# Kernel optimization log

Hardware: AMD Instinct MI355X
Metric: run time of the kernel (lower is better)

## Reference

```python
import jax, jax.numpy as jnp
import numpy as np

D_MODEL, D_HEAD, D_MLP, N_HEADS = 768, 64, 3072, 12
BATCH, SEQ = 1, 4096
LN_EPS = 1e-05
IGNORE = -100000.0


def setup_inputs() -> dict:
    key = jax.random.key(0)
    ks = jax.random.split(key, 8)
    s = 0.02
    return {
        "resid_pre": jax.random.normal(ks[0], (BATCH, SEQ, D_MODEL), jnp.float32),
        "ln1_w": jnp.ones((D_MODEL,), jnp.float32),
        "ln1_b": jnp.zeros((D_MODEL,), jnp.float32),
        "ln2_w": jnp.ones((D_MODEL,), jnp.float32),
        "ln2_b": jnp.zeros((D_MODEL,), jnp.float32),
        "W_Q": jax.random.normal(ks[1], (N_HEADS, D_MODEL, D_HEAD), jnp.float32) * s,
        "W_K": jax.random.normal(ks[2], (N_HEADS, D_MODEL, D_HEAD), jnp.float32) * s,
        "W_V": jax.random.normal(ks[3], (N_HEADS, D_MODEL, D_HEAD), jnp.float32) * s,
        "W_O": jax.random.normal(ks[4], (N_HEADS, D_HEAD, D_MODEL), jnp.float32) * s,
        "b_Q": jnp.zeros((N_HEADS, D_HEAD), jnp.float32),
        "b_K": jnp.zeros((N_HEADS, D_HEAD), jnp.float32),
        "b_V": jnp.zeros((N_HEADS, D_HEAD), jnp.float32),
        "b_O": jnp.zeros((D_MODEL,), jnp.float32),
        "W_in": jax.random.normal(ks[5], (D_MODEL, D_MLP), jnp.float32) * s,
        "b_in": jnp.zeros((D_MLP,), jnp.float32),
        "W_out": jax.random.normal(ks[6], (D_MLP, D_MODEL), jnp.float32) * s,
        "b_out": jnp.zeros((D_MODEL,), jnp.float32),
    }


def _layernorm(x, w, b):
    mean = jnp.mean(x, axis=-1, keepdims=True)
    var = jnp.var(x, axis=-1, keepdims=True)  # unbiased=False
    return (x - mean) * jax.lax.rsqrt(var + LN_EPS) * w + b


def _attention(x, W_Q, W_K, W_V, W_O, b_Q, b_K, b_V, b_O):
    # x: [b, s, d_model]; W_{Q,K,V}: [h, d_model, d_head]
    q = jnp.einsum("bsm,hmd->bshd", x, W_Q) + b_Q
    k = jnp.einsum("bsm,hmd->bshd", x, W_K) + b_K
    v = jnp.einsum("bsm,hmd->bshd", x, W_V) + b_V
    scores = jnp.einsum("bqhd,bkhd->bhqk", q, k) / np.sqrt(D_HEAD).astype(np.float32)
    seq = x.shape[1]
    causal = jnp.tril(jnp.ones((seq, seq), bool))  # True where allowed
    scores = jnp.where(causal, scores, IGNORE)
    pattern = jax.nn.softmax(scores, axis=-1)
    z = jnp.einsum("bkhd,bhqk->bqhd", v, pattern)
    return jnp.einsum("bqhd,hdm->bqm", z, W_O) + b_O


def reference(resid_pre, ln1_w, ln1_b, ln2_w, ln2_b,
              W_Q, W_K, W_V, W_O, b_Q, b_K, b_V, b_O,
              W_in, b_in, W_out, b_out):
    resid_mid = _attention(_layernorm(resid_pre, ln1_w, ln1_b),
                           W_Q, W_K, W_V, W_O, b_Q, b_K, b_V, b_O) + resid_pre
    pre = jnp.einsum("bsm,mf->bsf", _layernorm(resid_mid, ln2_w, ln2_b), W_in) + b_in
    post = jax.nn.gelu(pre, approximate=False)  # torch F.gelu default = exact erf
    mlp_out = jnp.einsum("bsf,fm->bsm", post, W_out) + b_out
    resid_post = mlp_out + resid_mid
    return (resid_post, post)
```

## Files before the change

kernel.cpp:

```cpp
#include <hip/hip_runtime.h>
#include <hip/hip_bf16.h>
#include <math.h>

using bf16 = __hip_bfloat16;
using u16  = unsigned short;
using u32  = unsigned int;
using short8 = __attribute__((ext_vector_type(8))) short;
using f32x4  = __attribute__((ext_vector_type(4))) float;

#define AS1 __attribute__((address_space(1)))
#define AS3 __attribute__((address_space(3)))

__device__ __forceinline__ void gld_lds16(const void* g, void* l) {
  __builtin_amdgcn_global_load_lds((const AS1 u32*)g, (AS3 u32*)l, 16, 0, 0);
}

__device__ __forceinline__ bool probe_f32(const void* p) {
  return *(const u32*)p == 0x3F800000u;
}
__device__ __forceinline__ float ldf(const void* p, size_t i, bool f32) {
  return f32 ? ((const float*)p)[i] : __bfloat162float(((const bf16*)p)[i]);
}
__device__ __forceinline__ void stf(void* p, size_t i, float v, bool f32) {
  if (f32) ((float*)p)[i] = v;
  else     ((bf16*)p)[i] = __float2bfloat16(v);
}
__device__ __forceinline__ u32 cvt_pk_bf16(float lo, float hi) {
  u32 r;
  asm("v_cvt_pk_bf16_f32 %0, %1, %2" : "=v"(r) : "v"(lo), "v"(hi));
  return r;
}

__global__ __launch_bounds__(256) void ln_kernel(const void* __restrict__ x,
    const void* __restrict__ w, const void* __restrict__ b, bf16* __restrict__ out,
    const void* probe, int x_is_f32)
{
  const bool pf = probe_f32(probe);
  const bool xf = x_is_f32 ? true : pf;
  const int row = blockIdx.x, t = threadIdx.x;
  const size_t base = (size_t)row * 768;
  float v[3]; float s1 = 0.f, s2 = 0.f;
#pragma unroll
  for (int i = 0; i < 3; ++i) { float f = ldf(x, base + i*256 + t, xf); v[i] = f; s1 += f; s2 += f*f; }
#pragma unroll
  for (int off = 32; off >= 1; off >>= 1) { s1 += __shfl_xor(s1, off); s2 += __shfl_xor(s2, off); }
  __shared__ float a1[4], a2[4];
  if ((t & 63) == 0) { a1[t>>6] = s1; a2[t>>6] = s2; }
  __syncthreads();
  float S1 = a1[0]+a1[1]+a1[2]+a1[3];
  float S2 = a2[0]+a2[1]+a2[2]+a2[3];
  float mean = S1 * (1.f/768.f);
  float var  = S2 * (1.f/768.f) - mean*mean;
  float rs = rsqrtf(var + 1e-5f);
#pragma unroll
  for (int i = 0; i < 3; ++i) {
    int c = i*256 + t;
    out[base + c] = __float2bfloat16((v[i]-mean)*rs*ldf(w, c, pf) + ldf(b, c, pf));
  }
}

__global__ __launch_bounds__(256) void prep_all(
    const void* W_Q, const void* W_K, const void* W_V, const void* Wo,
    const void* Win, const void* Wout,
    const void* bQ, const void* bK, const void* bV, const void* bO,
    const void* bIn, const void* bOut,
    bf16* __restrict__ qkvT, bf16* __restrict__ WoT, bf16* __restrict__ WinT,
    bf16* __restrict__ WoutT, float* __restrict__ biasA,
    const void* __restrict__ xres, bf16* __restrict__ lnout, const void* probe)
{
  const bool pf = probe_f32(probe);
  const int bid = blockIdx.x;
  const int t = threadIdx.x;
  if (bid >= 6939) {
    const int row = bid - 6939;
    const size_t base = (size_t)row * 768;
    float v[3]; float s1 = 0.f, s2 = 0.f;
#pragma unroll
    for (int i = 0; i < 3; ++i) { float f = ldf(xres, base + i*256 + t, pf); v[i] = f; s1 += f; s2 += f*f; }
#pragma unroll
    for (int off = 32; off >= 1; off >>= 1) { s1 += __shfl_xor(s1, off); s2 += __shfl_xor(s2, off); }
    __shared__ float a1[4], a2[4];
    if ((t & 63) == 0) { a1[t>>6] = s1; a2[t>>6] = s2; }
    __syncthreads();
    float S1 = a1[0]+a1[1]+a1[2]+a1[3];
    float S2 = a2[0]+a2[1]+a2[2]+a2[3];
    float mean = S1 * (1.f/768.f);
    float var  = S2 * (1.f/768.f) - mean*mean;
    float rs = rsqrtf(var + 1e-5f);
#pragma unroll
    for (int i = 0; i < 3; ++i)
      lnout[base + i*256 + t] = __float2bfloat16((v[i]-mean)*rs);
    return;
  }
  if (bid >= 6912) {
    int i = (bid - 6912)*256 + t;
    float v;
    if (i < 2304)      v = (i < 768) ? ldf(bQ, i, pf) : (i < 1536 ? ldf(bK, i-768, pf) : ldf(bV, i-1536, pf));
    else if (i < 3072) v = ldf(bO, i-2304, pf);
    else if (i < 6144) v = ldf(bIn, i-3072, pf);
    else               v = ldf(bOut, i-6144, pf);
    biasA[i] = v;
    return;
  }
  const void* src; bf16* dst; int R, C, bx, by; size_t soff = 0;
  if (bid < 1728) {
    int mtx = bid / 576, within = bid % 576;
    int h = within / 48, tt = within % 48;
    by = tt >> 1; bx = tt & 1;
    src = (mtx == 0) ? W_Q : (mtx == 1 ? W_K : W_V);
    soff = (size_t)h * 49152;
    dst = qkvT + ((size_t)mtx*768 + h*64) * 768;
    R = 768; C = 64;
  } else if (bid < 2304) {
    int within = bid - 1728; bx = within % 24; by = within / 24;
    src = Wo; dst = WoT; R = 768; C = 768;
  } else if (bid < 4608) {
    int within = bid - 2304; bx = within % 96; by = within / 96;
    src = Win; dst = WinT; R = 768; C = 3072;
  } else {
    int within = bid - 4608; bx = within % 24; by = within / 24;
    src = Wout; dst = WoutT; R = 3072; C = 768;
  }
  __shared__ bf16 tile[32][33];
  const int bc = bx*32, br = by*32;
  const int tx = t & 31, ty = t >> 5;
#pragma unroll
  for (int i = 0; i < 32; i += 8)
    tile[ty+i][tx] = __float2bfloat16(ldf(src, soff + (size_t)(br+ty+i)*C + bc + tx, pf));
  __syncthreads();
#pragma unroll
  for (int i = 0; i < 32; i += 8)
    dst[(size_t)(bc+ty+i)*R + br + tx] = tile[tx][ty+i];
}


template<int MODE, int BM, int BN, int BK>
__global__ __launch_bounds__(256) void gemm_bt(const bf16* __restrict__ A,
    const bf16* __restrict__ BT, const float* __restrict__ bias,
    const void* __restrict__ res, void* __restrict__ Cout, bf16* __restrict__ aux,
    size_t outOff, const void* probe, int M, int N, int K,
    float* __restrict__ zf, float* __restrict__ sf)
{
  constexpr int MR = BM/32, NR = BN/32;
  constexpr int CH = BK/8;
  __shared__ bf16 Alds[BM*BK];
  __shared__ bf16 Blds[BN*BK];
  const int tid = threadIdx.x;
  const int lane = tid & 63, w = tid >> 6;
  const int l15 = lane & 15, l4 = lane >> 4;

  if (MODE == 0) {
    int bid = blockIdx.y * gridDim.x + blockIdx.x;
    float4 z4 = {0.f, 0.f, 0.f, 0.f};
    float4* zp = (float4*)zf + (size_t)bid*1024;
#pragma unroll
    for (int i = 0; i < 4; ++i) zp[i*256 + tid] = z4;
    if (tid < 16) ((float4*)sf)[bid*16 + tid] = z4;
  }

  const int brow = blockIdx.y * BM, bcol = blockIdx.x * BN;
  const int wr = (w >> 1) * (BM/2), wc = (w & 1) * (BN/2);
  const bf16* Ag = A  + (size_t)brow * K;
  const bf16* Bg = BT + (size_t)bcol * K;
  f32x4 acc[MR][NR];
#pragma unroll
  for (int i = 0; i < MR; ++i)
#pragma unroll
    for (int j = 0; j < NR; ++j) acc[i][j] = 0.f;

  for (int kt = 0; kt < K; kt += BK) {
#pragma unroll
    for (int i = 0; i < BM*CH/256; ++i) {
      int id = i*256 + tid, r = id / CH, cc = id % CH;
      int sw = (r ^ (r >> 3)) & 7;
      gld_lds16(Ag + (size_t)r*K + kt + ((cc ^ sw) * 8), (char*)Alds + id*16);
    }
#pragma unroll
    for (int i = 0; i < BN*CH/256; ++i) {
      int id = i*256 + tid, r = id / CH, cc = id % CH;
      int sw = (r ^ (r >> 3)) & 7;
      gld_lds16(Bg + (size_t)r*K + kt + ((cc ^ sw) * 8), (char*)Blds + id*16);
    }
    __syncthreads();
#pragma unroll
    for (int kk = 0; kk < BK/32; ++kk) {
      short8 a[MR], b[NR];
#pragma unroll
      for (int mi = 0; mi < MR; ++mi) {
        int row = wr + mi*16 + l15, sw = (row ^ (row >> 3)) & 7;
        a[mi] = *(const short8*)((const char*)Alds + row*(BK*2) + (((kk*4 + l4) ^ sw) << 4));
      }
#pragma unroll
      for (int ni = 0; ni < NR; ++ni) {
        int row = wc + ni*16 + l15, sw = (row ^ (row >> 3)) & 7;
        b[ni] = *(const short8*)((const char*)Blds + row*(BK*2) + (((kk*4 + l4) ^ sw) << 4));
      }
      __builtin_amdgcn_s_setprio(1);
#pragma unroll
      for (int mi = 0; mi < MR; ++mi)
#pragma unroll
        for (int ni = 0; ni < NR; ++ni)
          acc[mi][ni] = __builtin_amdgcn_mfma_f32_16x16x32_bf16(a[mi], b[ni], acc[mi][ni], 0, 0, 0);
      __builtin_amdgcn_s_setprio(0);
    }
    __syncthreads();
  }

  const bool pf = probe_f32(probe);
#pragma unroll
  for (int mi = 0; mi < MR; ++mi) {
#pragma unroll
    for (int r = 0; r < 4; ++r) {
      int row = brow + wr + mi*16 + l4*4 + r;
      size_t rowoff = (size_t)row * N;
#pragma unroll
      for (int ni = 0; ni < NR; ++ni) {
        int col = bcol + wc + ni*16 + l15;
        float v = acc[mi][ni][r] + bias[col];
        if (MODE == 1) v += ldf(res, rowoff + col, pf);
        if (MODE == 3) v += ((const float*)res)[rowoff + col];
        if (MODE == 2) v = 0.5f * v * (1.0f + erff(v * 0.70710678118654752f));
        if (MODE == 0) ((bf16*)Cout)[rowoff + col] = __float2bfloat16(v);
        else if (MODE == 1) ((float*)Cout)[rowoff + col] = v;
        else {
          stf(Cout, outOff + rowoff + col, v, pf);
          if (MODE == 2) aux[rowoff + col] = __float2bfloat16(v);
        }
      }
    }
  }
}

__global__ __launch_bounds__(256) void attn_kernel(const bf16* __restrict__ QKV,
    float* __restrict__ Zf, float* __restrict__ Sf)
{
  __shared__ bf16 Ks[2][4096];
  __shared__ bf16 VTs[2][4096];
  __shared__ bf16 Ps[4][1024];
  const int cid = 159 - blockIdx.x, h = blockIdx.y;
  int qb, c;
  if (cid < 16)      { qb = cid;                    c = 0; }
  else if (cid < 48) { qb = 16 + ((cid-16) >> 1);   c = (cid-16) & 1; }
  else if (cid < 96) { qb = 32 + (cid-48)/3;        c = (cid-48)%3; }
  else               { qb = 48 + ((cid-96) >> 2);   c = (cid-96) & 3; }
  const int t_lo = c*16, t_hi = min(c*16 + 16, qb + 1);

  const int tid = threadIdx.x, lane = tid & 63, w = tid >> 6;
  const int l15 = lane & 15, l4 = lane >> 4;
  const int q0 = qb * 64;

  short8 qf[2];
#pragma unroll
  for (int kk = 0; kk < 2; ++kk)
    qf[kk] = *(const short8*)(QKV + (size_t)(q0 + w*16 + l15)*2304 + h*64 + kk*32 + l4*8);

  int kaddr[2][4], vaddr[2][4], pst[4], pld[2], vwa[8];
#pragma unroll
  for (int kk = 0; kk < 2; ++kk)
#pragma unroll
    for (int ct = 0; ct < 4; ++ct) {
      int krow = ct*16 + l15, sk = (krow ^ (krow >> 3)) & 7;
      kaddr[kk][ct] = krow*128 + (((kk*4 + l4) ^ sk) << 4);
      vaddr[kk][ct] = kaddr[kk][ct];
    }
#pragma unroll
  for (int r = 0; r < 4; ++r) {
    int prow = l4*4 + r, sp = (prow ^ (prow >> 3)) & 7;
    pst[r] = prow*128 + (((l15 >> 1) ^ sp) << 4) + (l15 & 1)*8;
  }
#pragma unroll
  for (int kg = 0; kg < 2; ++kg) {
    int sp2 = (l15 ^ (l15 >> 3)) & 7;
    pld[kg] = l15*128 + (((kg*4 + l4) ^ sp2) << 4);
  }
  const int vw = tid >> 3, vd0 = (tid & 7) * 8;
  const int vk0 = (vw >> 1) + (vw & 1) * 32;
#pragma unroll
  for (int d = 0; d < 8; ++d) {
    int row = vd0 + d, srow = (row ^ (row >> 3)) & 7;
    vwa[d] = row*128 + (((vw >> 2) ^ srow) << 4) + (vw & 3)*4;
  }

  const ptrdiff_t STEP = 64*2304;
  int id0 = tid, r0 = id0 >> 3;
  int s0 = (r0 ^ (r0 >> 3)) & 7, c0 = ((id0 & 7) ^ s0) * 8;
  int id1 = 256 + tid, r1 = id1 >> 3;
  int s1 = (r1 ^ (r1 >> 3)) & 7, c1 = ((id1 & 7) ^ s1) * 8;
  const bf16* kgp0 = QKV + (size_t)(t_lo*64 + r0)*2304 + 768 + h*64 + c0;
  const bf16* kgp1 = QKV + (size_t)(t_lo*64 + r1)*2304 + 768 + h*64 + c1;
  const int ksd0 = id0*16, ksd1 = id1*16;
  const bf16* vgp0 = QKV + (size_t)(t_lo*64 + vk0)*2304 + 1536 + h*64 + vd0;
  const bf16* vgp1 = vgp0 + (size_t)16*2304;
  uint4 va, vb;

  gld_lds16(kgp0, (char*)Ks[0] + ksd0);  kgp0 += STEP;
  gld_lds16(kgp1, (char*)Ks[0] + ksd1);  kgp1 += STEP;
  va = *(const uint4*)vgp0;  vgp0 += STEP;
  vb = *(const uint4*)vgp1;  vgp1 += STEP;
  {
    const u16* pa = (const u16*)&va; const u16* pb = (const u16*)&vb;
#pragma unroll
    for (int d = 0; d < 8; ++d)
      *(u32*)((char*)VTs[0] + vwa[d]) = (u32)pa[d] | ((u32)pb[d] << 16);
  }
  __syncthreads();

  f32x4 o[4]; f32x4 osum;
#pragma unroll
  for (int dt = 0; dt < 4; ++dt) o[dt] = 0.f;
  osum = 0.f;
  short8 ones8;
#pragma unroll
  for (int j = 0; j < 8; ++j) ones8[j] = 0x3F80;

#define ABODY(CUR, NT) {                                                        \
    const int nt_ = (NT);                                                       \
    const bool pref_ = (nt_ + 1 < t_hi);                                        \
    if (pref_) {                                                                \
      gld_lds16(kgp0, (char*)Ks[0] + ksd0 + ((CUR)^1)*8192);  kgp0 += STEP;     \
      gld_lds16(kgp1, (char*)Ks[0] + ksd1 + ((CUR)^1)*8192);  kgp1 += STEP;     \
      va = *(const uint4*)vgp0;  vgp0 += STEP;                                  \
      vb = *(const uint4*)vgp1;  vgp1 += STEP;                                  \
    }                                                                           \
    f32x4 s4[4];                                                                \
    _Pragma("unroll") for (int ct = 0; ct < 4; ++ct) s4[ct] = 0.f;              \
    __builtin_amdgcn_s_setprio(1);                                              \
    _Pragma("unroll") for (int kk = 0; kk < 2; ++kk)                            \
      _Pragma("unroll") for (int ct = 0; ct < 4; ++ct) {                        \
        short8 bk = *(const short8*)((const char*)Ks[0] + kaddr[kk][ct] + (CUR)*8192); \
        s4[ct] = __builtin_amdgcn_mfma_f32_16x16x32_bf16(qf[kk], bk, s4[ct], 0, 0, 0); \
      }                                                                         \
    __builtin_amdgcn_s_setprio(0);                                              \
    const bool diag_ = (nt_ == qb);                                             \
    _Pragma("unroll") for (int r = 0; r < 4; ++r) {                             \
      float p_[4];                                                              \
      _Pragma("unroll") for (int ct = 0; ct < 4; ++ct) {                        \
        float sv = s4[ct][r] * 0.18033688f;                                     \
        if (diag_ && (ct*16 + l15 > w*16 + l4*4 + r)) sv = -30000.0f;           \
        p_[ct] = exp2f(fminf(sv, 43.0f));                                       \
      }                                                                         \
      uint2 pk;                                                                 \
      pk.x = cvt_pk_bf16(p_[0], p_[1]);                                         \
      pk.y = cvt_pk_bf16(p_[2], p_[3]);                                         \
      *(uint2*)((char*)&Ps[w][0] + pst[r]) = pk;                                \
    }                                                                           \
    __builtin_amdgcn_s_setprio(1);                                              \
    _Pragma("unroll") for (int kg = 0; kg < 2; ++kg) {                          \
      short8 ap = *(const short8*)((const char*)&Ps[w][0] + pld[kg]);           \
      _Pragma("unroll") for (int dt = 0; dt < 4; ++dt) {                        \
        short8 bv = *(const short8*)((const char*)VTs[0] + vaddr[kg][dt] + (CUR)*8192); \
        o[dt] = __builtin_amdgcn_mfma_f32_16x16x32_bf16(ap, bv, o[dt], 0, 0, 0); \
      }                                                                         \
      osum = __builtin_amdgcn_mfma_f32_16x16x32_bf16(ap, ones8, osum, 0, 0, 0); \
    }                                                                           \
    __builtin_amdgcn_s_setprio(0);                                              \
    if (pref_) {                                                                \
      const u16* pa_ = (const u16*)&va; const u16* pb_ = (const u16*)&vb;       \
      _Pragma("unroll") for (int d = 0; d < 8; ++d)                             \
        *(u32*)((char*)VTs[0] + vwa[d] + ((CUR)^1)*8192) = (u32)pa_[d] | ((u32)pb_[d] << 16); \
    }                                                                           \
    __syncthreads();                                                            \
  }

  const int n = t_hi - t_lo;
  int j2 = 0;
  for (; j2 + 2 <= n; j2 += 2) {
    ABODY(0, t_lo + j2);
    ABODY(1, t_lo + j2 + 1);
  }
  if (j2 < n) ABODY(0, t_lo + j2);
#undef ABODY

  const int qrow0 = q0 + w*16 + l4*4;
#pragma unroll
  for (int r = 0; r < 4; ++r)
    if (l15 == 0) unsafeAtomicAdd(&Sf[(size_t)h*4096 + qrow0 + r], osum[r]);
#pragma unroll
  for (int dt = 0; dt < 4; ++dt)
#pragma unroll
    for (int r = 0; r < 4; ++r)
      unsafeAtomicAdd(&Zf[(size_t)(qrow0 + r)*768 + h*64 + dt*16 + l15], o[dt][r]);
}

__global__ __launch_bounds__(256) void norm_z(const float* __restrict__ Zf,
    const float* __restrict__ Sf, bf16* __restrict__ Zb)
{
  const int row = blockIdx.x, t = threadIdx.x;
  const size_t base = (size_t)row * 768;
#pragma unroll
  for (int i = 0; i < 3; ++i) {
    int cx = i*256 + t;
    int hh = cx >> 6;
    Zb[base + cx] = __float2bfloat16(Zf[base + cx] * __builtin_amdgcn_rcpf(Sf[(size_t)hh*4096 + row]));
  }
}

extern "C" void kernel_launch(void* const* d_in, const int* in_sizes, int n_in,
                              void* d_out, int out_size, void* d_ws, size_t ws_size,
                              hipStream_t stream)
{
  (void)in_sizes; (void)n_in; (void)out_size; (void)ws_size;
  const void* resid_pre = d_in[0];
  const void* ln1_w = d_in[1];
  const void* ln1_b = d_in[2];
  const void* ln2_w = d_in[3];
  const void* ln2_b = d_in[4];
  const void* W_Q  = d_in[5];
  const void* W_K  = d_in[6];
  const void* W_V  = d_in[7];
  const void* W_O  = d_in[8];
  const void* b_Q  = d_in[9];
  const void* b_K  = d_in[10];
  const void* b_V  = d_in[11];
  const void* b_O  = d_in[12];
  const void* W_in  = d_in[13];
  const void* b_in  = d_in[14];
  const void* W_out = d_in[15];
  const void* b_out = d_in[16];
  const void* probe = ln1_w;

  char* ws = (char*)d_ws;
  bf16*  qkvT  = (bf16*)(ws + 0);
  bf16*  WoT   = (bf16*)(ws + 3538944);
  bf16*  WinT  = (bf16*)(ws + 4718592);
  bf16*  WoutT = (bf16*)(ws + 9437184);
  float* biasA = (float*)(ws + 14155776);
  bf16*  x1    = (bf16*)(ws + 14183424);
  bf16*  QKV   = (bf16*)(ws + 20474880);
  bf16*  Zb    = (bf16*)(ws + 39349248);
  float* mid   = (float*)(ws + 45640704);
  bf16*  x2    = (bf16*)(ws + 58223616);
  bf16*  postB = (bf16*)(ws + 20474880);
  float* Zf    = (float*)(ws + 45640704);
  float* Sf    = (float*)(ws + 58223616);

  prep_all<<<6939, 256, 0, stream>>>(W_Q, W_K, W_V, W_O, W_in, W_out,
      b_Q, b_K, b_V, b_O, b_in, b_out, qkvT, WoT, WinT, WoutT, biasA,
      resid_pre, x1, probe);

  ln_kernel<<<4096, 256, 0, stream>>>(resid_pre, ln1_w, ln1_b, x1, probe, 0);
  gemm_bt<0,128,96,64><<<dim3(24,32), 256, 0, stream>>>(x1, qkvT, biasA, nullptr, QKV, nullptr, 0, probe, 4096, 2304, 768, Zf, Sf);
  attn_kernel<<<dim3(160,12), 256, 0, stream>>>(QKV, Zf, Sf);
  norm_z<<<4096, 256, 0, stream>>>(Zf, Sf, Zb);
  gemm_bt<1,64,64,128><<<dim3(12,64), 256, 0, stream>>>(Zb, WoT, biasA+2304, resid_pre, mid, nullptr, 0, probe, 4096, 768, 768, nullptr, nullptr);
  ln_kernel<<<4096, 256, 0, stream>>>(mid, ln2_w, ln2_b, x2, probe, 1);
  gemm_bt<2,128,128,64><<<dim3(24,32), 256, 0, stream>>>(x2, WinT, biasA+3072, nullptr, d_out, postB, 3145728, probe, 4096, 3072, 768, nullptr, nullptr);
  gemm_bt<3,64,64,128><<<dim3(12,64), 256, 0, stream>>>(postB, WoutT, biasA+6144, mid, d_out, nullptr, 0, probe, 4096, 768, 3072, nullptr, nullptr);
}
```

Baseline: 229.1 us.

## Fold LN1 into prep kernel and stage K via registers

The prep kernel grid grows to cover 4096 extra blocks that compute the first layernorm with weight and bias applied, and the separate LN1 launch is removed. Before, the prep blocks doing this work were never launched, so ln_kernel did it. In attention, K tiles are now loaded into registers and written to LDS after the PV MFMAs, the same way V is staged, instead of using direct global-to-LDS loads. The redundant vaddr array is dropped in favour of kaddr. The aim is to save one kernel launch and to overlap K load latency with compute, at the cost of extra VGPRs and explicit LDS stores.

```diff
diff --git a/kernel.cpp b/kernel.cpp
--- a/kernel.cpp
+++ b/kernel.cpp
@@ -66,7 +66,8 @@
     const void* bIn, const void* bOut,
     bf16* __restrict__ qkvT, bf16* __restrict__ WoT, bf16* __restrict__ WinT,
     bf16* __restrict__ WoutT, float* __restrict__ biasA,
-    const void* __restrict__ xres, bf16* __restrict__ lnout, const void* probe)
+    const void* __restrict__ xres, const void* lw, const void* lb,
+    bf16* __restrict__ lnout, const void* probe)
 {
   const bool pf = probe_f32(probe);
   const int bid = blockIdx.x;
@@ -88,8 +89,10 @@
     float var  = S2 * (1.f/768.f) - mean*mean;
     float rs = rsqrtf(var + 1e-5f);
 #pragma unroll
-    for (int i = 0; i < 3; ++i)
-      lnout[base + i*256 + t] = __float2bfloat16((v[i]-mean)*rs);
+    for (int i = 0; i < 3; ++i) {
+      int c = i*256 + t;
+      lnout[base + c] = __float2bfloat16((v[i]-mean)*rs*ldf(lw, c, pf) + ldf(lb, c, pf));
+    }
     return;
   }
   if (bid >= 6912) {
@@ -133,7 +136,6 @@
     dst[(size_t)(bc+ty+i)*R + br + tx] = tile[tx][ty+i];
 }
 
-
 template<int MODE, int BM, int BN, int BK>
 __global__ __launch_bounds__(256) void gemm_bt(const bf16* __restrict__ A,
     const bf16* __restrict__ BT, const float* __restrict__ bias,
@@ -254,14 +256,13 @@
   for (int kk = 0; kk < 2; ++kk)
     qf[kk] = *(const short8*)(QKV + (size_t)(q0 + w*16 + l15)*2304 + h*64 + kk*32 + l4*8);
 
-  int kaddr[2][4], vaddr[2][4], pst[4], pld[2], vwa[8];
+  int kaddr[2][4], pst[4], pld[2], vwa[8];
 #pragma unroll
   for (int kk = 0; kk < 2; ++kk)
 #pragma unroll
     for (int ct = 0; ct < 4; ++ct) {
       int krow = ct*16 + l15, sk = (krow ^ (krow >> 3)) & 7;
       kaddr[kk][ct] = krow*128 + (((kk*4 + l4) ^ sk) << 4);
-      vaddr[kk][ct] = kaddr[kk][ct];
     }
 #pragma unroll
   for (int r = 0; r < 4; ++r) {
@@ -291,12 +292,14 @@
   const int ksd0 = id0*16, ksd1 = id1*16;
   const bf16* vgp0 = QKV + (size_t)(t_lo*64 + vk0)*2304 + 1536 + h*64 + vd0;
   const bf16* vgp1 = vgp0 + (size_t)16*2304;
-  uint4 va, vb;
-
-  gld_lds16(kgp0, (char*)Ks[0] + ksd0);  kgp0 += STEP;
-  gld_lds16(kgp1, (char*)Ks[0] + ksd1);  kgp1 += STEP;
+  uint4 va, vb, ka, kb;
+
+  ka = *(const uint4*)kgp0;  kgp0 += STEP;
+  kb = *(const uint4*)kgp1;  kgp1 += STEP;
   va = *(const uint4*)vgp0;  vgp0 += STEP;
   vb = *(const uint4*)vgp1;  vgp1 += STEP;
+  *(uint4*)((char*)Ks[0] + ksd0) = ka;
+  *(uint4*)((char*)Ks[0] + ksd1) = kb;
   {
     const u16* pa = (const u16*)&va; const u16* pb = (const u16*)&vb;
 #pragma unroll
@@ -317,8 +320,8 @@
     const int nt_ = (NT);                                                       \
     const bool pref_ = (nt_ + 1 < t_hi);                                        \
     if (pref_) {                                                                \
-      gld_lds16(kgp0, (char*)Ks[0] + ksd0 + ((CUR)^1)*8192);  kgp0 += STEP;     \
-      gld_lds16(kgp1, (char*)Ks[0] + ksd1 + ((CUR)^1)*8192);  kgp1 += STEP;     \
+      ka = *(const uint4*)kgp0;  kgp0 += STEP;                                  \
+      kb = *(const uint4*)kgp1;  kgp1 += STEP;                                  \
       va = *(const uint4*)vgp0;  vgp0 += STEP;                                  \
       vb = *(const uint4*)vgp1;  vgp1 += STEP;                                  \
     }                                                                           \
@@ -348,13 +351,15 @@
     _Pragma("unroll") for (int kg = 0; kg < 2; ++kg) {                          \
       short8 ap = *(const short8*)((const char*)&Ps[w][0] + pld[kg]);           \
       _Pragma("unroll") for (int dt = 0; dt < 4; ++dt) {                        \
-        short8 bv = *(const short8*)((const char*)VTs[0] + vaddr[kg][dt] + (CUR)*8192); \
+        short8 bv = *(const short8*)((const char*)VTs[0] + kaddr[kg][dt] + (CUR)*8192); \
         o[dt] = __builtin_amdgcn_mfma_f32_16x16x32_bf16(ap, bv, o[dt], 0, 0, 0); \
       }                                                                         \
       osum = __builtin_amdgcn_mfma_f32_16x16x32_bf16(ap, ones8, osum, 0, 0, 0); \
     }                                                                           \
     __builtin_amdgcn_s_setprio(0);                                              \
     if (pref_) {                                                                \
+      *(uint4*)((char*)Ks[0] + ksd0 + ((CUR)^1)*8192) = ka;                     \
+      *(uint4*)((char*)Ks[0] + ksd1 + ((CUR)^1)*8192) = kb;                     \
       const u16* pa_ = (const u16*)&va; const u16* pb_ = (const u16*)&vb;       \
       _Pragma("unroll") for (int d = 0; d < 8; ++d)                             \
         *(u32*)((char*)VTs[0] + vwa[d] + ((CUR)^1)*8192) = (u32)pa_[d] | ((u32)pb_[d] << 16); \
@@ -434,11 +439,10 @@
   float* Zf    = (float*)(ws + 45640704);
   float* Sf    = (float*)(ws + 58223616);
 
-  prep_all<<<6939, 256, 0, stream>>>(W_Q, W_K, W_V, W_O, W_in, W_out,
+  prep_all<<<11035, 256, 0, stream>>>(W_Q, W_K, W_V, W_O, W_in, W_out,
       b_Q, b_K, b_V, b_O, b_in, b_out, qkvT, WoT, WinT, WoutT, biasA,
-      resid_pre, x1, probe);
-
-  ln_kernel<<<4096, 256, 0, stream>>>(resid_pre, ln1_w, ln1_b, x1, probe, 0);
+      resid_pre, ln1_w, ln1_b, x1, probe);
+
   gemm_bt<0,128,96,64><<<dim3(24,32), 256, 0, stream>>>(x1, qkvT, biasA, nullptr, QKV, nullptr, 0, probe, 4096, 2304, 768, Zf, Sf);
   attn_kernel<<<dim3(160,12), 256, 0, stream>>>(QKV, Zf, Sf);
   norm_z<<<4096, 256, 0, stream>>>(Zf, Sf, Zb);
```

Result: no change. 225.3 us (-1.6%).
